# Performance work log

Measured on AMD Instinct MI355X. Metric: run time of the kernel, lower is better.

Reference implementation:

```python
import jax, jax.numpy as jnp
import numpy as np

HIDDEN = 1024
B, S = 64, 512

def setup_inputs() -> dict:
    key = jax.random.key(0)
    k1, k2, k3, k4, k5 = jax.random.split(key, 5)
    hidden = jax.random.normal(k1, (2, B, HIDDEN), dtype=jnp.float32)
    encoder_outputs = jax.random.normal(k2, (B, S, HIDDEN), dtype=jnp.float32)
    # nn.Linear(3H, H): weight [H, 3H], bias [H]
    bound = 1.0 / np.sqrt(3 * HIDDEN)
    W = jax.random.uniform(k3, (HIDDEN, 3 * HIDDEN), dtype=jnp.float32, minval=-bound, maxval=bound)
    b = jax.random.uniform(k4, (HIDDEN,), dtype=jnp.float32, minval=-bound, maxval=bound)
    v = jax.random.normal(k5, (HIDDEN,), dtype=jnp.float32)
    return {"hidden": hidden, "encoder_outputs": encoder_outputs, "W": W, "b": b, "v": v}

def reference(hidden, encoder_outputs, W, b, v):
    # hidden: [2, B, H]; encoder_outputs: [B, S, H]
    B_, S_, H = encoder_outputs.shape
    # concat the two decoder layers -> [B, 2H], broadcast over seq
    hidden2 = jnp.concatenate([hidden[0], hidden[1]], axis=1)  # [B, 2H]
    hidden2 = jnp.broadcast_to(hidden2[:, None, :], (B_, S_, 2 * H))
    attn_input = jnp.concatenate([hidden2, encoder_outputs], axis=2)  # [B, S, 3H]
    energy = jnp.einsum('bsk,hk->bsh', attn_input, W) + b  # [B, S, H]
    scores = jnp.einsum('bsh,h->bs', energy, v)  # [B, S]
    # original softmaxes over the seq axis (dim 0 of [S, B]), then transposes -> [B, S]
    return jax.nn.softmax(scores, axis=1)
```

## Files before the change

kernel.cpp:

```cpp
#include <hip/hip_runtime.h>


#define HID 1024
#define BB  64
#define SS  512
#define W3H 3072

typedef float floatx4 __attribute__((ext_vector_type(4)));

__global__ __launch_bounds__(1024) void wfold_kernel(
        const float* __restrict__ W, const float* __restrict__ v,
        float* __restrict__ w2) {
    __shared__ float part[64][16];
    const int kl = threadIdx.x & 15;
    const int hg = threadIdx.x >> 4;
    const int k  = blockIdx.x * 16 + kl;
    float acc = 0.0f;
    #pragma unroll
    for (int h = hg * 16; h < hg * 16 + 16; ++h)
        acc += v[h] * W[(size_t)h * W3H + 2 * HID + k];
    part[hg][kl] = acc;
    __syncthreads();
    for (int half = 32; half >= 1; half >>= 1) {
        if (hg < half) part[hg][kl] += part[hg + half][kl];
        __syncthreads();
    }
    if (threadIdx.x < 16) w2[k] = part[0][kl];
}

__global__ __launch_bounds__(256) void scores_kernel(
        const floatx4* __restrict__ enc4, const floatx4* __restrict__ w24,
        float* __restrict__ scores) {
    const int wave = threadIdx.x >> 6;
    const int lane = threadIdx.x & 63;
    const int r = blockIdx.x * 4 + wave;
    const floatx4* row = enc4 + (size_t)r * (HID / 4);
    float acc = 0.0f;
    #pragma unroll
    for (int i = 0; i < 4; ++i) {
        floatx4 e = __builtin_nontemporal_load(&row[i * 64 + lane]);
        floatx4 w = w24[i * 64 + lane];
        acc += e.x * w.x + e.y * w.y + e.z * w.z + e.w * w.w;
    }
    #pragma unroll
    for (int off = 32; off > 0; off >>= 1)
        acc += __shfl_down(acc, off);
    if (lane == 0) scores[r] = acc;
}

__global__ __launch_bounds__(512) void softmax_kernel(
        const float* __restrict__ scores, float* __restrict__ out) {
    __shared__ float red[8];
    const int b = blockIdx.x;
    const int t = threadIdx.x;
    const int wave = t >> 6, lane = t & 63;

    float x = scores[b * SS + t];

    float m = x;
    #pragma unroll
    for (int off = 32; off > 0; off >>= 1)
        m = fmaxf(m, __shfl_down(m, off));
    if (lane == 0) red[wave] = m;
    __syncthreads();
    if (t == 0) {
        float mm = red[0];
        #pragma unroll
        for (int i = 1; i < 8; ++i) mm = fmaxf(mm, red[i]);
        red[0] = mm;
    }
    __syncthreads();
    m = red[0];
    __syncthreads();

    float e = expf(x - m);

    float s = e;
    #pragma unroll
    for (int off = 32; off > 0; off >>= 1)
        s += __shfl_down(s, off);
    if (lane == 0) red[wave] = s;
    __syncthreads();
    if (t == 0) {
        float tot = 0.0f;
        #pragma unroll
        for (int i = 0; i < 8; ++i) tot += red[i];
        red[0] = tot;
    }
    __syncthreads();
    out[b * SS + t] = e / red[0];
}

extern "C" void kernel_launch(void* const* d_in, const int* in_sizes, int n_in,
                              void* d_out, int out_size, void* d_ws, size_t ws_size,
                              hipStream_t stream) {
    const float* enc = (const float*)d_in[1];
    const float* W   = (const float*)d_in[2];
    const float* v   = (const float*)d_in[4];
    float* out = (float*)d_out;

    float* w2     = (float*)d_ws;
    float* scores = w2 + HID;

    wfold_kernel<<<64, 1024, 0, stream>>>(W, v, w2);

    scores_kernel<<<(BB * SS) / 4, 256, 0, stream>>>(
        (const floatx4*)enc, (const floatx4*)w2, scores);

    softmax_kernel<<<BB, 512, 0, stream>>>(scores, out);
}
```

Baseline: 199.4 us.

## Fuse softmax into scores kernel via last-block atomic counter per batch

Removes the separate softmax launch. Each scores block increments a per-batch atomic counter after writing its scores, and the 128th block to finish for a batch runs that batch's softmax over all 512 scores. The counters are reset inside the weight-fold kernel. This saves a kernel launch and its dependency gap, at the cost of an atomic and an extra barrier in every block, plus a serialized tail softmax done by the last block.

```diff
diff --git a/kernel.cpp b/kernel.cpp
--- a/kernel.cpp
+++ b/kernel.cpp
@@ -10,7 +10,8 @@
 
 __global__ __launch_bounds__(1024) void wfold_kernel(
         const float* __restrict__ W, const float* __restrict__ v,
-        float* __restrict__ w2) {
+        float* __restrict__ w2, unsigned* __restrict__ cnt) {
+    if (threadIdx.x == 0) cnt[blockIdx.x] = 0u;
     __shared__ float part[64][16];
     const int kl = threadIdx.x & 15;
     const int hg = threadIdx.x >> 4;
@@ -28,12 +29,14 @@
     if (threadIdx.x < 16) w2[k] = part[0][kl];
 }
 
-__global__ __launch_bounds__(256) void scores_kernel(
+__global__ __launch_bounds__(256) void scores_softmax_kernel(
         const floatx4* __restrict__ enc4, const floatx4* __restrict__ w24,
-        float* __restrict__ scores) {
+        float* __restrict__ scores, unsigned* __restrict__ cnt,
+        float* __restrict__ out) {
     const int wave = threadIdx.x >> 6;
     const int lane = threadIdx.x & 63;
     const int r = blockIdx.x * 4 + wave;
+    const int b = blockIdx.x >> 7;
     const floatx4* row = enc4 + (size_t)r * (HID / 4);
     float acc = 0.0f;
     #pragma unroll
@@ -46,49 +49,44 @@
     for (int off = 32; off > 0; off >>= 1)
         acc += __shfl_down(acc, off);
     if (lane == 0) scores[r] = acc;
-}
 
-__global__ __launch_bounds__(512) void softmax_kernel(
-        const float* __restrict__ scores, float* __restrict__ out) {
-    __shared__ float red[8];
-    const int b = blockIdx.x;
+    __shared__ int isLast;
+    __syncthreads();
+    if (threadIdx.x == 0) {
+        unsigned old = __hip_atomic_fetch_add(&cnt[b], 1u,
+                          __ATOMIC_ACQ_REL, __HIP_MEMORY_SCOPE_AGENT);
+        isLast = (old == 127u);
+    }
+    __syncthreads();
+    if (!isLast) return;
+
     const int t = threadIdx.x;
-    const int wave = t >> 6, lane = t & 63;
+    float s0 = __hip_atomic_load(&scores[b * SS + t],
+                    __ATOMIC_RELAXED, __HIP_MEMORY_SCOPE_AGENT);
+    float s1 = __hip_atomic_load(&scores[b * SS + 256 + t],
+                    __ATOMIC_RELAXED, __HIP_MEMORY_SCOPE_AGENT);
 
-    float x = scores[b * SS + t];
-
-    float m = x;
+    __shared__ float red[4];
+    float m = fmaxf(s0, s1);
     #pragma unroll
     for (int off = 32; off > 0; off >>= 1)
         m = fmaxf(m, __shfl_down(m, off));
     if (lane == 0) red[wave] = m;
     __syncthreads();
-    if (t == 0) {
-        float mm = red[0];
-        #pragma unroll
-        for (int i = 1; i < 8; ++i) mm = fmaxf(mm, red[i]);
-        red[0] = mm;
-    }
-    __syncthreads();
-    m = red[0];
+    m = fmaxf(fmaxf(red[0], red[1]), fmaxf(red[2], red[3]));
     __syncthreads();
 
-    float e = expf(x - m);
-
-    float s = e;
+    float e0 = expf(s0 - m), e1 = expf(s1 - m);
+    float s = e0 + e1;
     #pragma unroll
     for (int off = 32; off > 0; off >>= 1)
         s += __shfl_down(s, off);
     if (lane == 0) red[wave] = s;
     __syncthreads();
-    if (t == 0) {
-        float tot = 0.0f;
-        #pragma unroll
-        for (int i = 0; i < 8; ++i) tot += red[i];
-        red[0] = tot;
-    }
-    __syncthreads();
-    out[b * SS + t] = e / red[0];
+    float tot = red[0] + red[1] + red[2] + red[3];
+
+    out[b * SS + t]       = e0 / tot;
+    out[b * SS + 256 + t] = e1 / tot;
 }
 
 extern "C" void kernel_launch(void* const* d_in, const int* in_sizes, int n_in,
@@ -99,13 +97,12 @@
     const float* v   = (const float*)d_in[4];
     float* out = (float*)d_out;
 
-    float* w2     = (float*)d_ws;
-    float* scores = w2 + HID;
+    float*    w2     = (float*)d_ws;
+    float*    scores = w2 + HID;
+    unsigned* cnt    = (unsigned*)(scores + BB * SS);
 
-    wfold_kernel<<<64, 1024, 0, stream>>>(W, v, w2);
+    wfold_kernel<<<64, 1024, 0, stream>>>(W, v, w2, cnt);
 
-    scores_kernel<<<(BB * SS) / 4, 256, 0, stream>>>(
-        (const floatx4*)enc, (const floatx4*)w2, scores);
-
-    softmax_kernel<<<BB, 512, 0, stream>>>(scores, out);
+    scores_softmax_kernel<<<(BB * SS) / 4, 256, 0, stream>>>(
+        (const floatx4*)enc, (const floatx4*)w2, scores, cnt, out);
 }
```

Result: slower. 569.5 us (+185.6%).
